# Performance work log

Hardware: AMD Instinct MI355X
Metric: run time of the kernel (lower is better)

The kernel has to match this reference:

```python
import jax, jax.numpy as jnp
import numpy as np

B, NS, NF, D, H = 64, 16, 4096, 128, 256  # batch, n_slots, n_feat, slot_dim, mlp_hidden
EPS_LN = 1e-5
EPS_ATT = 1e-8


def _layernorm(x, g, b):
    mu = x.mean(-1, keepdims=True)
    var = x.var(-1, keepdims=True)
    return (x - mu) / jnp.sqrt(var + EPS_LN) * g + b


def setup_inputs() -> dict:
    key = jax.random.key(0)
    ks = jax.random.split(key, 8)
    s = 0.02  # init scale for weights
    return {
        "t": jnp.zeros((), jnp.float32),
        "slots": jax.random.normal(ks[0], (B, NS, D), jnp.float32),
        "k": jax.random.normal(ks[1], (B, NF, D), jnp.float32),
        "v": jax.random.normal(ks[2], (B, NF, D), jnp.float32),
        "Wq": jax.random.normal(ks[3], (D, D), jnp.float32) * s,           # eqx Linear weight [out,in], no bias
        "ln_slots_g": jnp.ones((D,), jnp.float32),
        "ln_slots_b": jnp.zeros((D,), jnp.float32),
        "W_ih": jax.random.normal(ks[4], (3 * D, D), jnp.float32) * s,     # GRUCell input weights
        "W_hh": jax.random.normal(ks[5], (3 * D, D), jnp.float32) * s,     # GRUCell hidden weights
        "b_ih": jnp.zeros((3 * D,), jnp.float32),
        "b_n": jnp.zeros((D,), jnp.float32),
        "ln_ff_g": jnp.ones((D,), jnp.float32),
        "ln_ff_b": jnp.zeros((D,), jnp.float32),
        "W0": jax.random.normal(ks[6], (H, D), jnp.float32) * s,
        "b0": jnp.zeros((H,), jnp.float32),
        "W1": jax.random.normal(ks[7], (D, H), jnp.float32) * s,
        "b1": jnp.zeros((D,), jnp.float32),
    }


def reference(t, slots, k, v, Wq, ln_slots_g, ln_slots_b,
              W_ih, W_hh, b_ih, b_n, ln_ff_g, ln_ff_b, W0, b0, W1, b1):
    scale = D ** (-0.5)
    # LayerNorm over slot features, then query projection
    slots_norm = _layernorm(slots, ln_slots_g, ln_slots_b)
    q = jnp.einsum('bnd,ed->bne', slots_norm, Wq)                    # [B,NS,D]
    # Doubly-normalized slot attention: softmax over slots (axis=1), renorm over features
    att_logits = jnp.einsum('bnd,bmd->bnm', q, k) * scale            # [B,NS,NF]
    att = jax.nn.softmax(att_logits, axis=1)
    att = att / (att.sum(axis=-1, keepdims=True) + EPS_ATT)
    attended = jnp.einsum('bnm,bmd->bnd', att, v)                    # [B,NS,D]
    # GRUCell (equinox semantics): gates order (reset, input, new)
    igates = jnp.einsum('bnd,ed->bne', attended, W_ih) + b_ih        # [B,NS,3D]
    hgates = jnp.einsum('bnd,ed->bne', slots, W_hh)                  # [B,NS,3D]
    ir, ii, inew = jnp.split(igates, 3, axis=-1)
    hr, hi, hnew = jnp.split(hgates, 3, axis=-1)
    reset = jax.nn.sigmoid(ir + hr)
    inp = jax.nn.sigmoid(ii + hi)
    new = jnp.tanh(inew + reset * (hnew + b_n))
    gru_out = new + inp * (slots - new)                              # [B,NS,D]
    # LayerNorm -> MLP residual
    gru_normed = _layernorm(gru_out, ln_ff_g, ln_ff_b)
    h = jax.nn.relu(jnp.einsum('bnd,hd->bnh', gru_normed, W0) + b0)
    h = jnp.einsum('bnh,dh->bnd', h, W1) + b1
    target = gru_out + h
    return target - slots
```

## Files before the change

### kernel.cpp

```cpp
#include <hip/hip_runtime.h>
#include <hip/hip_bf16.h>
#include <math.h>

#define B_  64
#define NS_ 16
#define NF_ 4096
#define D_  128
#define H_  256


__device__ __forceinline__ float bflo(unsigned int u) { return __uint_as_float(u << 16); }
__device__ __forceinline__ float bfhi(unsigned int u) { return __uint_as_float(u & 0xffff0000u); }

__device__ __forceinline__ unsigned int pk_bf16(float a, float b) {
    unsigned int ua = __float_as_uint(a), ub = __float_as_uint(b);
    ua = (ua + 0x7FFFu + ((ua >> 16) & 1u)) >> 16;
    ub = (ub + 0x7FFFu + ((ub >> 16) & 1u)) >> 16;
    return ua | (ub << 16);
}

__device__ __forceinline__ float dot2_bf16(unsigned int a, unsigned int b, float c) {
    float d;
    asm("v_dot2_f32_bf16 %0, %1, %2, %3" : "=v"(d) : "v"(a), "v"(b), "v"(c));
    return d;
}

__device__ __forceinline__ float dot4(float4 a, float4 b) {
    return a.x * b.x + a.y * b.y + a.z * b.z + a.w * b.w;
}

__global__ __launch_bounds__(128) void k_q(
    const float* __restrict__ slots, const float* __restrict__ Wq,
    const float* __restrict__ lng, const float* __restrict__ lnb,
    unsigned int* __restrict__ q_out, float* __restrict__ acc, float* __restrict__ den) {
    const int b = blockIdx.x;
    const int t = threadIdx.x;
    __shared__ float sl_s[16][128];
    __shared__ float norm_s[16][128];
    __shared__ float st_s[16][8][2];
    __shared__ float mu_s[16], rs_s[16];
    __shared__ float q_s[16][128];

    const float4* sp = (const float4*)(slots + (size_t)b * 2048);
#pragma unroll
    for (int i = 0; i < 4; ++i) {
        int f = i * 128 + t;
        *(float4*)&sl_s[f >> 5][(f & 31) * 4] = sp[f];
    }
    __syncthreads();

    {
        int n = t >> 3, j = t & 7;
        float s1 = 0.f, s2 = 0.f;
#pragma unroll
        for (int d2 = 0; d2 < 16; ++d2) {
            float x = sl_s[n][j * 16 + d2];
            s1 += x; s2 += x * x;
        }
        st_s[n][j][0] = s1; st_s[n][j][1] = s2;
    }
    __syncthreads();
    if (t < 16) {
        float s1 = 0.f, s2 = 0.f;
#pragma unroll
        for (int j = 0; j < 8; ++j) { s1 += st_s[t][j][0]; s2 += st_s[t][j][1]; }
        float mu = s1 * (1.0f / 128.0f);
        float var = s2 * (1.0f / 128.0f) - mu * mu;
        mu_s[t] = mu;
        rs_s[t] = rsqrtf(var + 1e-5f);
    }
    __syncthreads();

    float gl = lng[t], bl = lnb[t];
#pragma unroll
    for (int n = 0; n < 16; ++n)
        norm_s[n][t] = (sl_s[n][t] - mu_s[n]) * rs_s[n] * gl + bl;
    __syncthreads();

    const float4* wq = (const float4*)(Wq + (size_t)t * 128);
    float qn[16];
#pragma unroll
    for (int n = 0; n < 16; ++n) qn[n] = 0.f;
#pragma unroll 4
    for (int j = 0; j < 32; ++j) {
        float4 w4 = wq[j];
#pragma unroll
        for (int n = 0; n < 16; ++n) qn[n] += dot4(w4, *(const float4*)&norm_s[n][4 * j]);
    }
#pragma unroll
    for (int n = 0; n < 16; ++n) q_s[n][t] = qn[n];

    float4 z4 = make_float4(0.f, 0.f, 0.f, 0.f);
    float4* ab = (float4*)(acc + (size_t)b * 2048);
#pragma unroll
    for (int i = 0; i < 4; ++i) ab[i * 128 + t] = z4;
    if (t < 16) den[b * 16 + t] = 0.f;
    __syncthreads();

    unsigned int* qo = q_out + (size_t)b * 1024;
#pragma unroll
    for (int i = 0; i < 8; ++i) {
        int u = i * 128 + t;
        int n = u >> 6, e2 = u & 63;
        qo[n * 64 + e2] = pk_bf16(q_s[n][2 * e2], q_s[n][2 * e2 + 1]);
    }
}

__global__ __launch_bounds__(256, 3) void k_attn(
    const float* __restrict__ kg_, const float* __restrict__ vg_,
    const unsigned int* __restrict__ q_u, float* __restrict__ acc_g, float* __restrict__ denom_g) {
    const int t = threadIdx.x;
    const int w = t >> 6, l = t & 63;
    const int b = blockIdx.y;
    const int n = l & 15;
    const int q4 = l >> 4;

    __shared__ unsigned int lds_u[9984];
    unsigned int* k_s = lds_u + w * 2496;
    unsigned int* v_s = k_s + 1088;
    float*        p_s = (float*)(k_s + 2176);

    uint4 qreg[16];
    {
        const uint4* qrow = (const uint4*)q_u + ((b * 16 + n) * 16);
#pragma unroll
        for (int jj = 0; jj < 16; ++jj) qreg[jj] = qrow[jj];
    }

    float accL[16], accH[16];
#pragma unroll
    for (int i = 0; i < 16; ++i) { accL[i] = 0.f; accH[i] = 0.f; }
    float denom_acc = 0.f;

    const size_t mbase = (size_t)b * NF_ + blockIdx.x * 256 + w * 64;
    const float4* kg4 = (const float4*)kg_ + mbase * 32;
    const float4* vg4 = (const float4*)vg_ + mbase * 32;

    uint2 kc[8], vc[8], kn2[8], vn2[8];
#pragma unroll
    for (int i = 0; i < 8; ++i) {
        float4 kk = kg4[i * 64 + l];
        float4 vv = vg4[i * 64 + l];
        kc[i] = make_uint2(pk_bf16(kk.x, kk.y), pk_bf16(kk.z, kk.w));
        vc[i] = make_uint2(pk_bf16(vv.x, vv.y), pk_bf16(vv.z, vv.w));
    }

    for (int tile = 0; tile < 4; ++tile) {
#pragma unroll
        for (int i = 0; i < 8; ++i) {
            int off = (2 * i + (l >> 5)) * 68 + 2 * (l & 31);
            *(uint2*)&k_s[off] = kc[i];
            *(uint2*)&v_s[off] = vc[i];
        }
        if (tile < 3) {
            const float4* kp = kg4 + (tile + 1) * 512;
            const float4* vp = vg4 + (tile + 1) * 512;
#pragma unroll
            for (int i = 0; i < 8; ++i) {
                float4 kk = kp[i * 64 + l];
                float4 vv = vp[i * 64 + l];
                kn2[i] = make_uint2(pk_bf16(kk.x, kk.y), pk_bf16(kk.z, kk.w));
                vn2[i] = make_uint2(pk_bf16(vv.x, vv.y), pk_bf16(vv.z, vv.w));
            }
        }

#pragma unroll
        for (int pass = 0; pass < 4; ++pass) {
            const int mi1 = pass * 4 + q4;
            float lg = 0.f;
#pragma unroll
            for (int jj = 0; jj < 16; ++jj) {
                uint4 kk = *(const uint4*)&k_s[mi1 * 68 + 4 * jj];
                lg = dot2_bf16(kk.x, qreg[jj].x, lg);
                lg = dot2_bf16(kk.y, qreg[jj].y, lg);
                lg = dot2_bf16(kk.z, qreg[jj].z, lg);
                lg = dot2_bf16(kk.w, qreg[jj].w, lg);
            }
            lg *= 0.08838834764831845f;
            float mx = lg;
            mx = fmaxf(mx, __shfl_xor(mx, 1));
            mx = fmaxf(mx, __shfl_xor(mx, 2));
            mx = fmaxf(mx, __shfl_xor(mx, 4));
            mx = fmaxf(mx, __shfl_xor(mx, 8));
            float e = __expf(lg - mx);
            float se = e;
            se += __shfl_xor(se, 1);
            se += __shfl_xor(se, 2);
            se += __shfl_xor(se, 4);
            se += __shfl_xor(se, 8);
            float pv = e / se;
            denom_acc += pv;
            p_s[mi1 * 20 + n] = pv;
        }

#pragma unroll 4
        for (int mi = 0; mi < 16; ++mi) {
            unsigned int vv2 = v_s[mi * 68 + l];
            float vlo = bflo(vv2), vhi = bfhi(vv2);
            float pv16[16];
            *(float4*)&pv16[0]  = *(const float4*)&p_s[mi * 20 + 0];
            *(float4*)&pv16[4]  = *(const float4*)&p_s[mi * 20 + 4];
            *(float4*)&pv16[8]  = *(const float4*)&p_s[mi * 20 + 8];
            *(float4*)&pv16[12] = *(const float4*)&p_s[mi * 20 + 12];
#pragma unroll
            for (int nn = 0; nn < 16; ++nn) {
                accL[nn] = fmaf(pv16[nn], vlo, accL[nn]);
                accH[nn] = fmaf(pv16[nn], vhi, accH[nn]);
            }
        }

#pragma unroll
        for (int i = 0; i < 8; ++i) { kc[i] = kn2[i]; vc[i] = vn2[i]; }
    }

    __syncthreads();
    float* red_f = (float*)lds_u;
    float* red_d = (float*)lds_u + 6144;
    red_d[t] = denom_acc;
    if (w > 0) {
#pragma unroll
        for (int nn = 0; nn < 16; ++nn)
            *(float2*)&red_f[(w - 1) * 2048 + nn * 128 + 2 * l] = make_float2(accL[nn], accH[nn]);
    }
    __syncthreads();
    if (w == 0) {
        float* base = acc_g + (size_t)(b * 16) * 128;
#pragma unroll
        for (int nn = 0; nn < 16; ++nn) {
            float2 r0 = *(const float2*)&red_f[0 * 2048 + nn * 128 + 2 * l];
            float2 r1 = *(const float2*)&red_f[1 * 2048 + nn * 128 + 2 * l];
            float2 r2 = *(const float2*)&red_f[2 * 2048 + nn * 128 + 2 * l];
            atomicAdd(base + nn * 128 + 2 * l,     accL[nn] + r0.x + r1.x + r2.x);
            atomicAdd(base + nn * 128 + 2 * l + 1, accH[nn] + r0.y + r1.y + r2.y);
        }
    }
    if (t < 16) {
        float s = 0.f;
#pragma unroll
        for (int j = 0; j < 16; ++j) s += red_d[t + 16 * j];
        atomicAdd(denom_g + b * 16 + t, s);
    }
}

__global__ __launch_bounds__(256) void k_final(
    const float* __restrict__ acc_g, const float* __restrict__ denom_g,
    const float* __restrict__ slots,
    const float* __restrict__ W_ih, const float* __restrict__ W_hh,
    const float* __restrict__ b_ih, const float* __restrict__ b_n,
    const float* __restrict__ ffg, const float* __restrict__ ffb,
    const float* __restrict__ W0, const float* __restrict__ b0,
    const float* __restrict__ W1, const float* __restrict__ b1,
    float* __restrict__ out) {
    const int bn0 = blockIdx.x * 4;
    const int t = threadIdx.x;
    __shared__ float att_s[4][128], slot_s[4][128];
    __shared__ float gates_s[4][4][128];
    __shared__ float gru_s[4][128], gn_s[4][128];
    __shared__ float h_s[4][256];

#pragma unroll
    for (int idx = t; idx < 512; idx += 256) {
        int bi = idx >> 7, d = idx & 127;
        int bn = bn0 + bi;
        float den = denom_g[bn] + 1e-8f;
        att_s[bi][d] = acc_g[(size_t)bn * 128 + d] / den;
        slot_s[bi][d] = slots[(size_t)bn * 128 + d];
    }
    __syncthreads();

    for (int g = t; g < 384; g += 256) {
        const float4* wi = (const float4*)(W_ih + (size_t)g * 128);
        const float4* wh = (const float4*)(W_hh + (size_t)g * 128);
        float si[4] = {0.f, 0.f, 0.f, 0.f}, sh[4] = {0.f, 0.f, 0.f, 0.f};
#pragma unroll 4
        for (int j = 0; j < 32; ++j) {
            float4 wi4 = wi[j], wh4 = wh[j];
#pragma unroll
            for (int bi = 0; bi < 4; ++bi) {
                si[bi] += dot4(wi4, *(const float4*)&att_s[bi][4 * j]);
                sh[bi] += dot4(wh4, *(const float4*)&slot_s[bi][4 * j]);
            }
        }
        float bih = b_ih[g];
        int d = g & 127;
#pragma unroll
        for (int bi = 0; bi < 4; ++bi) {
            if (g < 128)       gates_s[bi][0][d] = si[bi] + sh[bi] + bih;
            else if (g < 256)  gates_s[bi][1][d] = si[bi] + sh[bi] + bih;
            else { gates_s[bi][2][d] = si[bi] + bih; gates_s[bi][3][d] = sh[bi]; }
        }
    }
    __syncthreads();

    {
        int bi = t >> 6, l = t & 63;
        float gr[2], s1 = 0.f, s2 = 0.f;
#pragma unroll
        for (int h = 0; h < 2; ++h) {
            int d = l + 64 * h;
            float rr = 1.f / (1.f + __expf(-gates_s[bi][0][d]));
            float ii = 1.f / (1.f + __expf(-gates_s[bi][1][d]));
            float nv = tanhf(gates_s[bi][2][d] + rr * (gates_s[bi][3][d] + b_n[d]));
            float gru = nv + ii * (slot_s[bi][d] - nv);
            gr[h] = gru;
            gru_s[bi][d] = gru;
            s1 += gru; s2 += gru * gru;
        }
#pragma unroll
        for (int m = 1; m < 64; m <<= 1) { s1 += __shfl_xor(s1, m); s2 += __shfl_xor(s2, m); }
        float mu = s1 * (1.0f / 128.0f);
        float var = s2 * (1.0f / 128.0f) - mu * mu;
        float rstd = rsqrtf(var + 1e-5f);
#pragma unroll
        for (int h = 0; h < 2; ++h) {
            int d = l + 64 * h;
            gn_s[bi][d] = (gr[h] - mu) * rstd * ffg[d] + ffb[d];
        }
    }
    __syncthreads();

    {
        const float4* w0 = (const float4*)(W0 + (size_t)t * 128);
        float s[4] = {0.f, 0.f, 0.f, 0.f};
#pragma unroll 4
        for (int j = 0; j < 32; ++j) {
            float4 w4 = w0[j];
#pragma unroll
            for (int bi = 0; bi < 4; ++bi) s[bi] += dot4(w4, *(const float4*)&gn_s[bi][4 * j]);
        }
        float b0v = b0[t];
#pragma unroll
        for (int bi = 0; bi < 4; ++bi) h_s[bi][t] = fmaxf(s[bi] + b0v, 0.f);
    }
    __syncthreads();

    {
        int dr = t & 127, bp = (t >> 7) * 2;
        const float4* w1 = (const float4*)(W1 + (size_t)dr * 256);
        float s[2] = {0.f, 0.f};
#pragma unroll 4
        for (int j = 0; j < 64; ++j) {
            float4 w4 = w1[j];
#pragma unroll
            for (int u = 0; u < 2; ++u) s[u] += dot4(w4, *(const float4*)&h_s[bp + u][4 * j]);
        }
        float b1v = b1[dr];
#pragma unroll
        for (int u = 0; u < 2; ++u) {
            int bi = bp + u;
            out[(size_t)(bn0 + bi) * 128 + dr] = gru_s[bi][dr] + s[u] + b1v - slot_s[bi][dr];
        }
    }
}

extern "C" void kernel_launch(void* const* d_in, const int* in_sizes, int n_in,
                              void* d_out, int out_size, void* d_ws, size_t ws_size,
                              hipStream_t stream) {
    const float* slots = (const float*)d_in[1];
    const float* k     = (const float*)d_in[2];
    const float* v     = (const float*)d_in[3];
    const float* Wq    = (const float*)d_in[4];
    const float* lng   = (const float*)d_in[5];
    const float* lnb   = (const float*)d_in[6];
    const float* W_ih  = (const float*)d_in[7];
    const float* W_hh  = (const float*)d_in[8];
    const float* b_ih  = (const float*)d_in[9];
    const float* b_n   = (const float*)d_in[10];
    const float* ffg   = (const float*)d_in[11];
    const float* ffb   = (const float*)d_in[12];
    const float* W0    = (const float*)d_in[13];
    const float* b0    = (const float*)d_in[14];
    const float* W1    = (const float*)d_in[15];
    const float* b1    = (const float*)d_in[16];

    char* ws = (char*)d_ws;
    unsigned int* q_u = (unsigned int*)ws;
    float* acc = (float*)(ws + 262144);
    float* den = (float*)(ws + 786432);

    k_q<<<dim3(B_), dim3(128), 0, stream>>>(slots, Wq, lng, lnb, q_u, acc, den);
    k_attn<<<dim3(16, B_), dim3(256), 0, stream>>>(k, v, q_u, acc, den);
    k_final<<<dim3(256), dim3(256), 0, stream>>>(acc, den, slots, W_ih, W_hh,
                                                 b_ih, b_n, ffg, ffb, W0, b0, W1, b1,
                                                 (float*)d_out);
}
```

Baseline: 431.0 us.

## Split attention logit dot across lane groups and stream V directly from global

```diff
diff --git a/kernel.cpp b/kernel.cpp
--- a/kernel.cpp
+++ b/kernel.cpp
@@ -106,25 +106,24 @@
     }
 }
 
-__global__ __launch_bounds__(256, 3) void k_attn(
+__global__ __launch_bounds__(256, 4) void k_attn(
     const float* __restrict__ kg_, const float* __restrict__ vg_,
     const unsigned int* __restrict__ q_u, float* __restrict__ acc_g, float* __restrict__ denom_g) {
     const int t = threadIdx.x;
     const int w = t >> 6, l = t & 63;
     const int b = blockIdx.y;
     const int n = l & 15;
-    const int q4 = l >> 4;
-
-    __shared__ unsigned int lds_u[9984];
-    unsigned int* k_s = lds_u + w * 2496;
-    unsigned int* v_s = k_s + 1088;
-    float*        p_s = (float*)(k_s + 2176);
-
-    uint4 qreg[16];
+    const int g = l >> 4;
+
+    __shared__ unsigned int lds_u[6400];
+    unsigned int* k_s = lds_u + w * 1344;
+    float*        p_s = (float*)(k_s + 1088);
+
+    uint4 qq[4];
     {
         const uint4* qrow = (const uint4*)q_u + ((b * 16 + n) * 16);
 #pragma unroll
-        for (int jj = 0; jj < 16; ++jj) qreg[jj] = qrow[jj];
+        for (int j = 0; j < 4; ++j) qq[j] = qrow[g * 4 + j];
     }
 
     float accL[16], accH[16];
@@ -132,85 +131,79 @@
     for (int i = 0; i < 16; ++i) { accL[i] = 0.f; accH[i] = 0.f; }
     float denom_acc = 0.f;
 
-    const size_t mbase = (size_t)b * NF_ + blockIdx.x * 256 + w * 64;
+    const size_t mbase = (size_t)b * NF_ + blockIdx.x * 128 + w * 32;
     const float4* kg4 = (const float4*)kg_ + mbase * 32;
-    const float4* vg4 = (const float4*)vg_ + mbase * 32;
-
-    uint2 kc[8], vc[8], kn2[8], vn2[8];
-#pragma unroll
-    for (int i = 0; i < 8; ++i) {
-        float4 kk = kg4[i * 64 + l];
-        float4 vv = vg4[i * 64 + l];
-        kc[i] = make_uint2(pk_bf16(kk.x, kk.y), pk_bf16(kk.z, kk.w));
-        vc[i] = make_uint2(pk_bf16(vv.x, vv.y), pk_bf16(vv.z, vv.w));
-    }
-
-    for (int tile = 0; tile < 4; ++tile) {
+    const float2* vg2 = (const float2*)vg_ + mbase * 64;
+
+    for (int tile = 0; tile < 2; ++tile) {
+        const float4* kp = kg4 + tile * 512;
 #pragma unroll
         for (int i = 0; i < 8; ++i) {
+            float4 kk = kp[i * 64 + l];
             int off = (2 * i + (l >> 5)) * 68 + 2 * (l & 31);
-            *(uint2*)&k_s[off] = kc[i];
-            *(uint2*)&v_s[off] = vc[i];
-        }
-        if (tile < 3) {
-            const float4* kp = kg4 + (tile + 1) * 512;
-            const float4* vp = vg4 + (tile + 1) * 512;
-#pragma unroll
-            for (int i = 0; i < 8; ++i) {
-                float4 kk = kp[i * 64 + l];
-                float4 vv = vp[i * 64 + l];
-                kn2[i] = make_uint2(pk_bf16(kk.x, kk.y), pk_bf16(kk.z, kk.w));
-                vn2[i] = make_uint2(pk_bf16(vv.x, vv.y), pk_bf16(vv.z, vv.w));
+            *(uint2*)&k_s[off] = make_uint2(pk_bf16(kk.x, kk.y), pk_bf16(kk.z, kk.w));
+        }
+
+#pragma unroll
+        for (int mi = 0; mi < 16; ++mi) {
+            float p0 = 0.f, p1 = 0.f, p2 = 0.f, p3 = 0.f;
+#pragma unroll
+            for (int j = 0; j < 4; ++j) {
+                uint4 kk = *(const uint4*)&k_s[mi * 68 + g * 16 + 4 * j];
+                p0 = dot2_bf16(kk.x, qq[j].x, p0);
+                p1 = dot2_bf16(kk.y, qq[j].y, p1);
+                p2 = dot2_bf16(kk.z, qq[j].z, p2);
+                p3 = dot2_bf16(kk.w, qq[j].w, p3);
             }
-        }
-
-#pragma unroll
-        for (int pass = 0; pass < 4; ++pass) {
-            const int mi1 = pass * 4 + q4;
-            float lg = 0.f;
-#pragma unroll
-            for (int jj = 0; jj < 16; ++jj) {
-                uint4 kk = *(const uint4*)&k_s[mi1 * 68 + 4 * jj];
-                lg = dot2_bf16(kk.x, qreg[jj].x, lg);
-                lg = dot2_bf16(kk.y, qreg[jj].y, lg);
-                lg = dot2_bf16(kk.z, qreg[jj].z, lg);
-                lg = dot2_bf16(kk.w, qreg[jj].w, lg);
-            }
-            lg *= 0.08838834764831845f;
-            float mx = lg;
-            mx = fmaxf(mx, __shfl_xor(mx, 1));
-            mx = fmaxf(mx, __shfl_xor(mx, 2));
-            mx = fmaxf(mx, __shfl_xor(mx, 4));
-            mx = fmaxf(mx, __shfl_xor(mx, 8));
-            float e = __expf(lg - mx);
+            float x = (p0 + p1) + (p2 + p3);
+            x += __shfl_xor(x, 16);
+            x += __shfl_xor(x, 32);
+            x *= 0.08838834764831845f;
+            float e = __expf(x);
             float se = e;
             se += __shfl_xor(se, 1);
             se += __shfl_xor(se, 2);
             se += __shfl_xor(se, 4);
             se += __shfl_xor(se, 8);
-            float pv = e / se;
-            denom_acc += pv;
-            p_s[mi1 * 20 + n] = pv;
-        }
-
-#pragma unroll 4
-        for (int mi = 0; mi < 16; ++mi) {
-            unsigned int vv2 = v_s[mi * 68 + l];
-            float vlo = bflo(vv2), vhi = bfhi(vv2);
-            float pv16[16];
-            *(float4*)&pv16[0]  = *(const float4*)&p_s[mi * 20 + 0];
-            *(float4*)&pv16[4]  = *(const float4*)&p_s[mi * 20 + 4];
-            *(float4*)&pv16[8]  = *(const float4*)&p_s[mi * 20 + 8];
-            *(float4*)&pv16[12] = *(const float4*)&p_s[mi * 20 + 12];
-#pragma unroll
-            for (int nn = 0; nn < 16; ++nn) {
-                accL[nn] = fmaf(pv16[nn], vlo, accL[nn]);
-                accH[nn] = fmaf(pv16[nn], vhi, accH[nn]);
+            float pv = e * __builtin_amdgcn_rcpf(se);
+            if (g == (mi & 3)) {
+                denom_acc += pv;
+                p_s[mi * 16 + n] = pv;
             }
         }
 
 #pragma unroll
-        for (int i = 0; i < 8; ++i) { kc[i] = kn2[i]; vc[i] = vn2[i]; }
+        for (int half = 0; half < 2; ++half) {
+            float2 v2r[8];
+#pragma unroll
+            for (int i = 0; i < 8; ++i)
+                v2r[i] = vg2[(size_t)(tile * 16 + half * 8 + i) * 64 + l];
+#pragma unroll
+            for (int i = 0; i < 8; ++i) {
+                int mi = half * 8 + i;
+                float vlo = v2r[i].x, vhi = v2r[i].y;
+                float4 pp0 = *(const float4*)&p_s[mi * 16 + 0];
+                float4 pp1 = *(const float4*)&p_s[mi * 16 + 4];
+                float4 pp2 = *(const float4*)&p_s[mi * 16 + 8];
+                float4 pp3 = *(const float4*)&p_s[mi * 16 + 12];
+                accL[0]  = fmaf(pp0.x, vlo, accL[0]);  accH[0]  = fmaf(pp0.x, vhi, accH[0]);
+                accL[1]  = fmaf(pp0.y, vlo, accL[1]);  accH[1]  = fmaf(pp0.y, vhi, accH[1]);
+                accL[2]  = fmaf(pp0.z, vlo, accL[2]);  accH[2]  = fmaf(pp0.z, vhi, accH[2]);
+                accL[3]  = fmaf(pp0.w, vlo, accL[3]);  accH[3]  = fmaf(pp0.w, vhi, accH[3]);
+                accL[4]  = fmaf(pp1.x, vlo, accL[4]);  accH[4]  = fmaf(pp1.x, vhi, accH[4]);
+                accL[5]  = fmaf(pp1.y, vlo, accL[5]);  accH[5]  = fmaf(pp1.y, vhi, accH[5]);
+                accL[6]  = fmaf(pp1.z, vlo, accL[6]);  accH[6]  = fmaf(pp1.z, vhi, accH[6]);
+                accL[7]  = fmaf(pp1.w, vlo, accL[7]);  accH[7]  = fmaf(pp1.w, vhi, accH[7]);
+                accL[8]  = fmaf(pp2.x, vlo, accL[8]);  accH[8]  = fmaf(pp2.x, vhi, accH[8]);
+                accL[9]  = fmaf(pp2.y, vlo, accL[9]);  accH[9]  = fmaf(pp2.y, vhi, accH[9]);
+                accL[10] = fmaf(pp2.z, vlo, accL[10]); accH[10] = fmaf(pp2.z, vhi, accH[10]);
+                accL[11] = fmaf(pp2.w, vlo, accL[11]); accH[11] = fmaf(pp2.w, vhi, accH[11]);
+                accL[12] = fmaf(pp3.x, vlo, accL[12]); accH[12] = fmaf(pp3.x, vhi, accH[12]);
+                accL[13] = fmaf(pp3.y, vlo, accL[13]); accH[13] = fmaf(pp3.y, vhi, accH[13]);
+                accL[14] = fmaf(pp3.z, vlo, accL[14]); accH[14] = fmaf(pp3.z, vhi, accH[14]);
+                accL[15] = fmaf(pp3.w, vlo, accL[15]); accH[15] = fmaf(pp3.w, vhi, accH[15]);
+            }
+        }
     }
 
     __syncthreads();
@@ -379,7 +372,7 @@
     float* den = (float*)(ws + 786432);
 
     k_q<<<dim3(B_), dim3(128), 0, stream>>>(slots, Wq, lng, lnb, q_u, acc, den);
-    k_attn<<<dim3(16, B_), dim3(256), 0, stream>>>(k, v, q_u, acc, den);
+    k_attn<<<dim3(32, B_), dim3(256), 0, stream>>>(k, v, q_u, acc, den);
     k_final<<<dim3(256), dim3(256), 0, stream>>>(acc, den, slots, W_ih, W_hh,
                                                  b_ih, b_n, ffg, ffb, W0, b0, W1, b1,
                                                  (float*)d_out);
```

After: 433.8 us. Within noise of the previous version (+0.7%).
